# Kernel tuning notes

Measured on AMD Instinct MI355X. Metric: run time of the kernel, lower is better.

Reference implementation:

```python
import jax, jax.numpy as jnp
import numpy as np

HQ, HK, D = 16, 4, 64
WINDOW = 1024  # sliding-window left size; right=0 (causal)
GATE_CH = 12
RMS_EPS = 1e-8


def rms_norm(x):
    return x * jax.lax.rsqrt(jnp.mean(x * x, axis=-1, keepdims=True) + RMS_EPS)


def apply_rope(x, cos, sin):
    # x: [B,T,H,D]; cos/sin: [T,D//2] broadcast to [1,T,1,D//2]
    x1, x2 = jnp.split(x, 2, axis=-1)
    c = cos[None, :, None, :]
    s = sin[None, :, None, :]
    return jnp.concatenate([x1 * c - x2 * s, x1 * s + x2 * c], axis=-1)


def setup_inputs() -> dict:
    key = jax.random.key(0)
    ks = jax.random.split(key, 7)
    B, T, E = 2, 2048, HQ * D
    x = jax.random.normal(ks[0], (B, T, E), jnp.float32)
    value_embeds = jax.random.normal(ks[1], (B, T, HK * D), jnp.float32)
    # rope cache: angles for half the head dim
    inv_freq = 1.0 / (10000.0 ** (jnp.arange(D // 2, dtype=jnp.float32) / (D // 2)))
    ang = jnp.arange(T, dtype=jnp.float32)[:, None] * inv_freq[None, :]
    rope_cos = jnp.cos(ang)
    rope_sin = jnp.sin(ang)
    std = (3.0 ** 0.5) * (E ** -0.5)
    w_qkv = jax.random.uniform(ks[2], ((HQ + 2 * HK) * D, E), jnp.float32, -std, std)
    w_gate = jax.random.normal(ks[3], (HK, GATE_CH), jnp.float32) * 0.02
    w_o = jax.random.normal(ks[4], (E, E), jnp.float32) * 0.02
    return {"x": x, "value_embeds": value_embeds, "rope_cos": rope_cos,
            "rope_sin": rope_sin, "w_qkv": w_qkv, "w_gate": w_gate, "w_o": w_o}


def reference(x, value_embeds, rope_cos, rope_sin, w_qkv, w_gate, w_o):
    B, T, E = x.shape
    groups = HQ // HK
    qkv = jnp.einsum('bte,fe->btf', x, w_qkv).reshape(B, T, HQ + 2 * HK, D)
    q = qkv[:, :, :HQ, :]
    k = qkv[:, :, HQ:HQ + HK, :]
    v = qkv[:, :, HQ + HK:, :]
    # value-embedding gating
    ve = value_embeds.reshape(B, T, HK, D)
    gate = 3.0 * jax.nn.sigmoid(jnp.einsum('btc,hc->bth', x[..., :GATE_CH], w_gate))
    v = v + gate[..., None] * ve
    # rope + qk-norm
    q = rms_norm(apply_rope(q, rope_cos, rope_sin))
    k = rms_norm(apply_rope(k, rope_cos, rope_sin))
    # GQA: repeat kv heads
    k_rep = jnp.repeat(k, groups, axis=2)  # [B,T,HQ,D]
    v_rep = jnp.repeat(v, groups, axis=2)
    scale = 1.0 / jnp.sqrt(jnp.float32(D))
    scores = jnp.einsum('bqhd,bkhd->bhqk', q, k_rep) * scale
    i = jnp.arange(T)[:, None]
    j = jnp.arange(T)[None, :]
    mask = (j <= i) & (j >= i - WINDOW)  # causal + sliding window
    scores = jnp.where(mask[None, None], scores, jnp.float32(-1e30))
    attn = jax.nn.softmax(scores, axis=-1)
    out = jnp.einsum('bhqk,bkhd->bqhd', attn, v_rep).reshape(B, T, E)
    out = jnp.einsum('bte,fe->btf', out, w_o)
    return out
```

## Files before the change

### kernel.cpp

```cpp
#include <hip/hip_runtime.h>
#include <math.h>

#define T_LEN 2048
#define NB 2
#define E_DIM 1024
#define F_DIM 1536
#define HQn 16
#define HKn 4
#define Dh 64
#define WIN 1024
#define GATE_CH 12
#define PS 72

typedef unsigned short u16;
typedef __attribute__((ext_vector_type(8))) short bf16x8;
typedef __attribute__((ext_vector_type(4))) short bf16x4;
typedef __attribute__((ext_vector_type(4))) float f32x4;

#if __has_builtin(__builtin_amdgcn_mfma_f32_16x16x16bf16_1k)
#define MFMA16(A, B, C) __builtin_amdgcn_mfma_f32_16x16x16bf16_1k(A, B, C, 0, 0, 0)
#elif __has_builtin(__builtin_amdgcn_mfma_f32_16x16x16_bf16)
#define MFMA16(A, B, C) __builtin_amdgcn_mfma_f32_16x16x16_bf16(A, B, C, 0, 0, 0)
#else
static __device__ __forceinline__ f32x4 mfma16_asm(bf16x4 a, bf16x4 b, f32x4 c) {
  f32x4 d;
  asm volatile("s_nop 1\n\tv_mfma_f32_16x16x16_bf16 %0, %1, %2, %3\n\ts_nop 7\n\ts_nop 7"
               : "=v"(d) : "v"(a), "v"(b), "v"(c));
  return d;
}
#define MFMA16(A, B, C) mfma16_asm(A, B, C)
#endif

__device__ __forceinline__ u16 f2bf(float f) {
  union { float f; unsigned int u; } v; v.f = f;
  unsigned int u = v.u + 0x7FFF + ((v.u >> 16) & 1);
  return (u16)(u >> 16);
}
__device__ __forceinline__ float bf2f(u16 h) {
  union { unsigned int u; float f; } v; v.u = ((unsigned int)h) << 16;
  return v.f;
}
__device__ __forceinline__ void async_copy16(const void* g, void* l) {
  __builtin_amdgcn_global_load_lds(
      (const __attribute__((address_space(1))) unsigned int*)g,
      (__attribute__((address_space(3))) unsigned int*)l, 16, 0, 0);
}

__global__ __launch_bounds__(256) void cvt_all(
    const float4* __restrict__ x, const float4* __restrict__ wqkv,
    const float4* __restrict__ wo, uint2* __restrict__ xb,
    uint2* __restrict__ wqb, uint2* __restrict__ wob)
{
  int blk = blockIdx.x;
  const float4* in; uint2* out; int i;
  if (blk < 4096)       { in = x;    out = xb;  i = blk * 256 + threadIdx.x; }
  else if (blk < 5632)  { in = wqkv; out = wqb; i = (blk - 4096) * 256 + threadIdx.x; }
  else                  { in = wo;   out = wob; i = (blk - 5632) * 256 + threadIdx.x; }
  float4 v = in[i];
  uint2 o;
  o.x = (unsigned)f2bf(v.x) | ((unsigned)f2bf(v.y) << 16);
  o.y = (unsigned)f2bf(v.z) | ((unsigned)f2bf(v.w) << 16);
  out[i] = o;
}

template<int STORE_BF16>
__global__ __launch_bounds__(256) void gemm_bf16(
    const u16* __restrict__ A, const u16* __restrict__ B,
    void* __restrict__ Cv, int M, int N, int K)
{
  __shared__ u16 As[128 * 32];
  __shared__ u16 Bs[128 * 32];
  const int tid = threadIdx.x;
  const int wave = tid >> 6, lane = tid & 63;
  const int quad = lane >> 4, lanelow = lane & 15;
  const int row0 = blockIdx.x * 128;
  const int col0 = blockIdx.y * 128;
  const int wm = (wave >> 1) * 64, wn = (wave & 1) * 64;

  f32x4 acc[4][4];
#pragma unroll
  for (int i = 0; i < 4; ++i)
#pragma unroll
    for (int j = 0; j < 4; ++j) acc[i][j] = (f32x4){0.f, 0.f, 0.f, 0.f};

  const int r1 = wave * 16 + (lane >> 2);
  const int c1 = (lane & 3) * 8;

  for (int k0 = 0; k0 < K; k0 += 32) {
    __syncthreads();
    async_copy16(A + (size_t)(row0 + r1) * K + k0 + c1,      &As[r1 * 32 + c1]);
    async_copy16(A + (size_t)(row0 + r1 + 64) * K + k0 + c1, &As[(r1 + 64) * 32 + c1]);
    async_copy16(B + (size_t)(col0 + r1) * K + k0 + c1,      &Bs[r1 * 32 + c1]);
    async_copy16(B + (size_t)(col0 + r1 + 64) * K + k0 + c1, &Bs[(r1 + 64) * 32 + c1]);
    __syncthreads();

    bf16x8 a[4], b[4];
#pragma unroll
    for (int i = 0; i < 4; ++i)
      a[i] = *(const bf16x8*)&As[(wm + i * 16 + lanelow) * 32 + quad * 8];
#pragma unroll
    for (int j = 0; j < 4; ++j)
      b[j] = *(const bf16x8*)&Bs[(wn + j * 16 + lanelow) * 32 + quad * 8];
#pragma unroll
    for (int i = 0; i < 4; ++i)
#pragma unroll
      for (int j = 0; j < 4; ++j)
        acc[i][j] = __builtin_amdgcn_mfma_f32_16x16x32_bf16(a[i], b[j], acc[i][j], 0, 0, 0);
  }

#pragma unroll
  for (int i = 0; i < 4; ++i)
#pragma unroll
    for (int j = 0; j < 4; ++j) {
      int r = row0 + wm + i * 16 + quad * 4;
      int c = col0 + wn + j * 16 + lanelow;
#pragma unroll
      for (int reg = 0; reg < 4; ++reg) {
        if (STORE_BF16)
          ((u16*)Cv)[(size_t)(r + reg) * N + c] = f2bf(acc[i][j][reg]);
        else
          ((float*)Cv)[(size_t)(r + reg) * N + c] = acc[i][j][reg];
      }
    }
}

__global__ __launch_bounds__(256) void postproc_bf(
    const u16* __restrict__ qkv, const float* __restrict__ x,
    const float* __restrict__ ve, const float* __restrict__ rcos,
    const float* __restrict__ rsin, const float* __restrict__ wg,
    u16* __restrict__ qa, u16* __restrict__ ka, u16* __restrict__ va)
{
  const int token = blockIdx.x;
  const int t = token & (T_LEN - 1);
  const int tid = threadIdx.x;
  const int wave = tid >> 6, lane = tid & 63;
  __shared__ float gate[HKn];
  if (tid < HKn) {
    float g = 0.f;
#pragma unroll
    for (int c = 0; c < GATE_CH; ++c)
      g += x[(size_t)token * E_DIM + c] * wg[tid * GATE_CH + c];
    gate[tid] = 3.f / (1.f + __expf(-g));
  }
  __syncthreads();
  const int half = lane & 31;
  for (int vi = wave; vi < HQn + HKn; vi += 4) {
    const u16* p = qkv + (size_t)token * F_DIM + vi * Dh;
    float c = rcos[t * 32 + half], s = rsin[t * 32 + half];
    float x1 = bf2f(p[half]), x2 = bf2f(p[half + 32]);
    float y = (lane < 32) ? (x1 * c - x2 * s) : (x1 * s + x2 * c);
    float ss = y * y;
#pragma unroll
    for (int o = 32; o; o >>= 1) ss += __shfl_xor(ss, o, 64);
    float v = y * rsqrtf(ss * (1.f / Dh) + 1e-8f);
    if (vi < HQn)
      qa[((size_t)token * HQn + vi) * Dh + lane] = f2bf(v * 0.1803368801f);
    else
      ka[((size_t)token * HKn + (vi - HQn)) * Dh + lane] = f2bf(v);
  }
  {
    float g = gate[tid >> 6];
    size_t vidx = (size_t)token * (HKn * Dh) + tid;
    va[vidx] = f2bf(bf2f(qkv[(size_t)token * F_DIM + (HQn + HKn) * Dh + tid]) + g * ve[vidx]);
  }
}

__global__ __launch_bounds__(256) void transpose_v(
    const u16* __restrict__ va, u16* __restrict__ vt)
{
  __shared__ u16 tile[64][PS];
  const int bhk = blockIdx.y;
  const int b = bhk >> 2, hk = bhk & 3;
  const int t0 = blockIdx.x * 64;
  const int tid = threadIdx.x;
#pragma unroll
  for (int p = 0; p < 2; ++p) {
    int s = tid + p * 256;
    int r = s >> 3, seg = s & 7;
    *(uint4*)&tile[r][seg * 8] =
        *(const uint4*)(va + ((size_t)(b * T_LEN + t0 + r) * HKn + hk) * Dh + seg * 8);
  }
  __syncthreads();
#pragma unroll
  for (int p = 0; p < 2; ++p) {
    int s = tid + p * 256;
    int d = s >> 3, seg = s & 7;
    u16 tmp[8];
#pragma unroll
    for (int e = 0; e < 8; ++e) tmp[e] = tile[seg * 8 + e][d];
    *(uint4*)(vt + ((size_t)bhk * Dh + d) * T_LEN + t0 + seg * 8) = *(uint4*)tmp;
  }
}

__global__ __launch_bounds__(256) void attn_mfma(
    const u16* __restrict__ qa, const u16* __restrict__ ka,
    const u16* __restrict__ vt_g, u16* __restrict__ att)
{
  __shared__ u16 Ks[2][64 * PS];
  __shared__ u16 Vt[2][64 * PS];
  const int qt = blockIdx.x, h = blockIdx.y, b = blockIdx.z;
  const int hk = h >> 2;
  const int qb = qt * 128;
  const int tid = threadIdx.x;
  const int wave = tid >> 6, lane = tid & 63;
  const int quad = lane >> 4, lanelow = lane & 15;

  bf16x8 aQ[2][2];
#pragma unroll
  for (int hh = 0; hh < 2; ++hh)
#pragma unroll
    for (int kk = 0; kk < 2; ++kk)
      aQ[hh][kk] = *(const bf16x8*)(qa +
          ((size_t)(b * T_LEN + qb + wave * 32 + hh * 16 + lanelow) * HQn + h) * Dh +
          kk * 32 + quad * 8);

  f32x4 O[4][2];
  float l[2] = {0.f, 0.f};
#pragma unroll
  for (int dt = 0; dt < 4; ++dt)
#pragma unroll
    for (int hh = 0; hh < 2; ++hh) O[dt][hh] = (f32x4){0.f, 0.f, 0.f, 0.f};

  const int i_lo = qb + wave * 32, i_hi = i_lo + 31;
  const int kt0 = (qt >= 8) ? qt * 2 - 16 : 0;
  const int kt1 = qt * 2 + 1;

  const int sr0 = tid >> 3,           sc0 = (tid & 7) * 8;
  const int sr1 = (tid + 256) >> 3,   sc1 = ((tid + 256) & 7) * 8;
  const u16* kg = ka + (size_t)(b * T_LEN) * (HKn * Dh) + hk * Dh;
  const u16* vg = vt_g + (size_t)(b * HKn + hk) * Dh * T_LEN;

  {
    const int kb = kt0 * 64;
    uint4 k0 = *(const uint4*)(kg + (size_t)(kb + sr0) * (HKn * Dh) + sc0);
    uint4 k1 = *(const uint4*)(kg + (size_t)(kb + sr1) * (HKn * Dh) + sc1);
    uint4 v0 = *(const uint4*)(vg + (size_t)sr0 * T_LEN + kb + sc0);
    uint4 v1 = *(const uint4*)(vg + (size_t)sr1 * T_LEN + kb + sc1);
    *(uint4*)&Ks[0][sr0 * PS + sc0] = k0;
    *(uint4*)&Ks[0][sr1 * PS + sc1] = k1;
    *(uint4*)&Vt[0][sr0 * PS + sc0] = v0;
    *(uint4*)&Vt[0][sr1 * PS + sc1] = v1;
  }

  for (int kt = kt0; kt <= kt1; ++kt) {
    const int buf = (kt - kt0) & 1;
    const int kb = kt * 64;
    uint4 k0, k1, v0, v1;
    const bool more = (kt < kt1);
    if (more) {
      const int nb = kb + 64;
      k0 = *(const uint4*)(kg + (size_t)(nb + sr0) * (HKn * Dh) + sc0);
      k1 = *(const uint4*)(kg + (size_t)(nb + sr1) * (HKn * Dh) + sc1);
      v0 = *(const uint4*)(vg + (size_t)sr0 * T_LEN + nb + sc0);
      v1 = *(const uint4*)(vg + (size_t)sr1 * T_LEN + nb + sc1);
    }
    __syncthreads();

    const bool active = (kb <= i_hi) && (kb + 63 >= i_lo - WIN);
    if (active) {
      f32x4 St[4][2];
#pragma unroll
      for (int jt = 0; jt < 4; ++jt) {
        bf16x8 aK0 = *(const bf16x8*)&Ks[buf][(jt * 16 + lanelow) * PS + quad * 8];
        bf16x8 aK1 = *(const bf16x8*)&Ks[buf][(jt * 16 + lanelow) * PS + 32 + quad * 8];
#pragma unroll
        for (int hh = 0; hh < 2; ++hh) {
          f32x4 acc = (f32x4){-12.f, -12.f, -12.f, -12.f};
          acc = __builtin_amdgcn_mfma_f32_16x16x32_bf16(aK0, aQ[hh][0], acc, 0, 0, 0);
          acc = __builtin_amdgcn_mfma_f32_16x16x32_bf16(aK1, aQ[hh][1], acc, 0, 0, 0);
          St[jt][hh] = acc;
        }
      }
      const bool need_mask = (kb + 63 > i_lo) || (kb < i_hi - WIN);
      if (need_mask) {
#pragma unroll
        for (int jt = 0; jt < 4; ++jt)
#pragma unroll
          for (int hh = 0; hh < 2; ++hh)
#pragma unroll
            for (int rr = 0; rr < 4; ++rr) {
              int ig = i_lo + hh * 16 + lanelow;
              int jg = kb + jt * 16 + quad * 4 + rr;
              if (jg > ig || jg < ig - WIN) St[jt][hh][rr] = -1e30f;
            }
      }
      bf16x4 Pt[4][2];
#pragma unroll
      for (int jt = 0; jt < 4; ++jt)
#pragma unroll
        for (int hh = 0; hh < 2; ++hh) {
          float p0 = __builtin_amdgcn_exp2f(St[jt][hh][0]);
          float p1 = __builtin_amdgcn_exp2f(St[jt][hh][1]);
          float p2 = __builtin_amdgcn_exp2f(St[jt][hh][2]);
          float p3 = __builtin_amdgcn_exp2f(St[jt][hh][3]);
          l[hh] += (p0 + p1) + (p2 + p3);
          bf16x4 pk;
          pk[0] = (short)f2bf(p0); pk[1] = (short)f2bf(p1);
          pk[2] = (short)f2bf(p2); pk[3] = (short)f2bf(p3);
          Pt[jt][hh] = pk;
        }
#pragma unroll
      for (int dt = 0; dt < 4; ++dt)
#pragma unroll
        for (int jt = 0; jt < 4; ++jt) {
          bf16x4 aV = *(const bf16x4*)&Vt[buf][(dt * 16 + lanelow) * PS + jt * 16 + quad * 4];
#pragma unroll
          for (int hh = 0; hh < 2; ++hh)
            O[dt][hh] = MFMA16(aV, Pt[jt][hh], O[dt][hh]);
        }
    }
    if (more) {
      const int nbuf = buf ^ 1;
      *(uint4*)&Ks[nbuf][sr0 * PS + sc0] = k0;
      *(uint4*)&Ks[nbuf][sr1 * PS + sc1] = k1;
      *(uint4*)&Vt[nbuf][sr0 * PS + sc0] = v0;
      *(uint4*)&Vt[nbuf][sr1 * PS + sc1] = v1;
    }
  }

#pragma unroll
  for (int hh = 0; hh < 2; ++hh) {
    float s = l[hh];
    s += __shfl_xor(s, 16, 64);
    s += __shfl_xor(s, 32, 64);
    float inv = 1.f / s;
    int qg = qb + wave * 32 + hh * 16 + lanelow;
    u16* obase = att + (size_t)(b * T_LEN + qg) * E_DIM + h * Dh;
#pragma unroll
    for (int dt = 0; dt < 4; ++dt) {
      bf16x4 ov;
      ov[0] = (short)f2bf(O[dt][hh][0] * inv);
      ov[1] = (short)f2bf(O[dt][hh][1] * inv);
      ov[2] = (short)f2bf(O[dt][hh][2] * inv);
      ov[3] = (short)f2bf(O[dt][hh][3] * inv);
      *(bf16x4*)(obase + dt * 16 + quad * 4) = ov;
    }
  }
}

extern "C" void kernel_launch(void* const* d_in, const int* in_sizes, int n_in,
                              void* d_out, int out_size, void* d_ws, size_t ws_size,
                              hipStream_t stream)
{
  const float* x    = (const float*)d_in[0];
  const float* ve   = (const float*)d_in[1];
  const float* rc   = (const float*)d_in[2];
  const float* rs   = (const float*)d_in[3];
  const float* wqkv = (const float*)d_in[4];
  const float* wg   = (const float*)d_in[5];
  const float* wo   = (const float*)d_in[6];
  float* out = (float*)d_out;

  char* ws = (char*)d_ws;
  u16* x_bf    = (u16*)(ws);
  u16* v_t     = x_bf;
  u16* wqkv_bf = (u16*)(ws + 8388608);
  u16* wo_bf   = (u16*)(ws + 11534336);
  u16* qkv_bf  = (u16*)(ws + 13631488);
  u16* att     = qkv_bf;
  u16* q_att   = (u16*)(ws + 26214400);
  u16* k_att   = (u16*)(ws + 34603008);
  u16* v_att   = (u16*)(ws + 36700160);

  cvt_all<<<6656, 256, 0, stream>>>((const float4*)x, (const float4*)wqkv,
                                    (const float4*)wo, (uint2*)x_bf,
                                    (uint2*)wqkv_bf, (uint2*)wo_bf);
  gemm_bf16<1><<<dim3(32, 12), 256, 0, stream>>>(x_bf, wqkv_bf, qkv_bf, 4096, F_DIM, E_DIM);
  postproc_bf<<<NB * T_LEN, 256, 0, stream>>>(qkv_bf, x, ve, rc, rs, wg, q_att, k_att, v_att);
  transpose_v<<<dim3(32, 8), 256, 0, stream>>>(v_att, v_t);
  attn_mfma<<<dim3(T_LEN / 128, HQn, NB), 256, 0, stream>>>(q_att, k_att, v_t, att);
  gemm_bf16<0><<<dim3(32, 8), 256, 0, stream>>>(att, wo_bf, out, 4096, E_DIM, E_DIM);
}
```

Baseline: 194.6 us.

## Shrink attention query tile to 64 and use smaller GEMM tiles for occupancy

```diff
diff --git a/kernel.cpp b/kernel.cpp
--- a/kernel.cpp
+++ b/kernel.cpp
@@ -13,6 +13,7 @@
 #define PS 72
 
 typedef unsigned short u16;
+typedef unsigned int u32;
 typedef __attribute__((ext_vector_type(8))) short bf16x8;
 typedef __attribute__((ext_vector_type(4))) short bf16x4;
 typedef __attribute__((ext_vector_type(4))) float f32x4;
@@ -40,6 +41,10 @@
   union { unsigned int u; float f; } v; v.u = ((unsigned int)h) << 16;
   return v.f;
 }
+__device__ __forceinline__ u32 pack_bf2(float hi, float lo) {
+  union { float f; u32 u; } a, b; a.f = hi; b.f = lo;
+  return __builtin_amdgcn_perm(a.u + 0x8000u, b.u + 0x8000u, 0x07060302u);
+}
 __device__ __forceinline__ void async_copy16(const void* g, void* l) {
   __builtin_amdgcn_global_load_lds(
       (const __attribute__((address_space(1))) unsigned int*)g,
@@ -63,55 +68,60 @@
   out[i] = o;
 }
 
-template<int STORE_BF16>
+template<int BM, int BN, int STORE_BF16>
 __global__ __launch_bounds__(256) void gemm_bf16(
     const u16* __restrict__ A, const u16* __restrict__ B,
     void* __restrict__ Cv, int M, int N, int K)
 {
-  __shared__ u16 As[128 * 32];
-  __shared__ u16 Bs[128 * 32];
+  constexpr int MI = BM / 32, NJ = BN / 32;
+  __shared__ u16 As[BM * 32];
+  __shared__ u16 Bs[BN * 32];
   const int tid = threadIdx.x;
   const int wave = tid >> 6, lane = tid & 63;
   const int quad = lane >> 4, lanelow = lane & 15;
-  const int row0 = blockIdx.x * 128;
-  const int col0 = blockIdx.y * 128;
-  const int wm = (wave >> 1) * 64, wn = (wave & 1) * 64;
-
-  f32x4 acc[4][4];
-#pragma unroll
-  for (int i = 0; i < 4; ++i)
-#pragma unroll
-    for (int j = 0; j < 4; ++j) acc[i][j] = (f32x4){0.f, 0.f, 0.f, 0.f};
+  const int row0 = blockIdx.x * BM;
+  const int col0 = blockIdx.y * BN;
+  const int wm = (wave >> 1) * (BM / 2), wn = (wave & 1) * (BN / 2);
+
+  f32x4 acc[MI][NJ];
+#pragma unroll
+  for (int i = 0; i < MI; ++i)
+#pragma unroll
+    for (int j = 0; j < NJ; ++j) acc[i][j] = (f32x4){0.f, 0.f, 0.f, 0.f};
 
   const int r1 = wave * 16 + (lane >> 2);
   const int c1 = (lane & 3) * 8;
 
   for (int k0 = 0; k0 < K; k0 += 32) {
     __syncthreads();
-    async_copy16(A + (size_t)(row0 + r1) * K + k0 + c1,      &As[r1 * 32 + c1]);
-    async_copy16(A + (size_t)(row0 + r1 + 64) * K + k0 + c1, &As[(r1 + 64) * 32 + c1]);
-    async_copy16(B + (size_t)(col0 + r1) * K + k0 + c1,      &Bs[r1 * 32 + c1]);
-    async_copy16(B + (size_t)(col0 + r1 + 64) * K + k0 + c1, &Bs[(r1 + 64) * 32 + c1]);
+#pragma unroll
+    for (int p = 0; p < BM / 64; ++p)
+      async_copy16(A + (size_t)(row0 + r1 + p * 64) * K + k0 + c1,
+                   &As[(r1 + p * 64) * 32 + c1]);
+#pragma unroll
+    for (int p = 0; p < BN / 64; ++p)
+      async_copy16(B + (size_t)(col0 + r1 + p * 64) * K + k0 + c1,
+                   &Bs[(r1 + p * 64) * 32 + c1]);
     __syncthreads();
 
-    bf16x8 a[4], b[4];
-#pragma unroll
-    for (int i = 0; i < 4; ++i)
+    bf16x8 a[MI], b[NJ];
+#pragma unroll
+    for (int i = 0; i < MI; ++i)
       a[i] = *(const bf16x8*)&As[(wm + i * 16 + lanelow) * 32 + quad * 8];
 #pragma unroll
-    for (int j = 0; j < 4; ++j)
+    for (int j = 0; j < NJ; ++j)
       b[j] = *(const bf16x8*)&Bs[(wn + j * 16 + lanelow) * 32 + quad * 8];
 #pragma unroll
-    for (int i = 0; i < 4; ++i)
-#pragma unroll
-      for (int j = 0; j < 4; ++j)
+    for (int i = 0; i < MI; ++i)
+#pragma unroll
+      for (int j = 0; j < NJ; ++j)
         acc[i][j] = __builtin_amdgcn_mfma_f32_16x16x32_bf16(a[i], b[j], acc[i][j], 0, 0, 0);
   }
 
 #pragma unroll
-  for (int i = 0; i < 4; ++i)
-#pragma unroll
-    for (int j = 0; j < 4; ++j) {
+  for (int i = 0; i < MI; ++i)
+#pragma unroll
+    for (int j = 0; j < NJ; ++j) {
       int r = row0 + wm + i * 16 + quad * 4;
       int c = col0 + wn + j * 16 + lanelow;
 #pragma unroll
@@ -200,33 +210,28 @@
   __shared__ u16 Vt[2][64 * PS];
   const int qt = blockIdx.x, h = blockIdx.y, b = blockIdx.z;
   const int hk = h >> 2;
-  const int qb = qt * 128;
+  const int qb = qt * 64;
   const int tid = threadIdx.x;
   const int wave = tid >> 6, lane = tid & 63;
   const int quad = lane >> 4, lanelow = lane & 15;
 
-  bf16x8 aQ[2][2];
-#pragma unroll
-  for (int hh = 0; hh < 2; ++hh)
-#pragma unroll
-    for (int kk = 0; kk < 2; ++kk)
-      aQ[hh][kk] = *(const bf16x8*)(qa +
-          ((size_t)(b * T_LEN + qb + wave * 32 + hh * 16 + lanelow) * HQn + h) * Dh +
-          kk * 32 + quad * 8);
-
-  f32x4 O[4][2];
-  float l[2] = {0.f, 0.f};
-#pragma unroll
-  for (int dt = 0; dt < 4; ++dt)
-#pragma unroll
-    for (int hh = 0; hh < 2; ++hh) O[dt][hh] = (f32x4){0.f, 0.f, 0.f, 0.f};
-
-  const int i_lo = qb + wave * 32, i_hi = i_lo + 31;
-  const int kt0 = (qt >= 8) ? qt * 2 - 16 : 0;
-  const int kt1 = qt * 2 + 1;
-
-  const int sr0 = tid >> 3,           sc0 = (tid & 7) * 8;
-  const int sr1 = (tid + 256) >> 3,   sc1 = ((tid + 256) & 7) * 8;
+  bf16x8 aQ[2];
+#pragma unroll
+  for (int kk = 0; kk < 2; ++kk)
+    aQ[kk] = *(const bf16x8*)(qa +
+        ((size_t)(b * T_LEN + qb + wave * 16 + lanelow) * HQn + h) * Dh +
+        kk * 32 + quad * 8);
+
+  f32x4 O[4];
+  float l = 0.f;
+#pragma unroll
+  for (int dt = 0; dt < 4; ++dt) O[dt] = (f32x4){0.f, 0.f, 0.f, 0.f};
+
+  const int kt0 = (qt >= 16) ? qt - 16 : 0;
+  const int kt1 = qt;
+
+  const int sr0 = tid >> 3,         sc0 = (tid & 7) * 8;
+  const int sr1 = (tid + 256) >> 3, sc1 = ((tid + 256) & 7) * 8;
   const u16* kg = ka + (size_t)(b * T_LEN) * (HKn * Dh) + hk * Dh;
   const u16* vg = vt_g + (size_t)(b * HKn + hk) * Dh * T_LEN;
 
@@ -256,59 +261,55 @@
     }
     __syncthreads();
 
-    const bool active = (kb <= i_hi) && (kb + 63 >= i_lo - WIN);
-    if (active) {
-      f32x4 St[4][2];
+    f32x4 St[4];
+#pragma unroll
+    for (int jt = 0; jt < 4; ++jt) {
+      bf16x8 aK0 = *(const bf16x8*)&Ks[buf][(jt * 16 + lanelow) * PS + quad * 8];
+      bf16x8 aK1 = *(const bf16x8*)&Ks[buf][(jt * 16 + lanelow) * PS + 32 + quad * 8];
+      f32x4 acc = (f32x4){-12.f, -12.f, -12.f, -12.f};
+      acc = __builtin_amdgcn_mfma_f32_16x16x32_bf16(aK0, aQ[0], acc, 0, 0, 0);
+      acc = __builtin_amdgcn_mfma_f32_16x16x32_bf16(aK1, aQ[1], acc, 0, 0, 0);
+      St[jt] = acc;
+    }
+    if (kt == kt1) {
+#pragma unroll
+      for (int jt = 0; jt < 4; ++jt)
+#pragma unroll
+        for (int rr = 0; rr < 4; ++rr) {
+          int ig = qb + wave * 16 + lanelow;
+          int jg = kb + jt * 16 + quad * 4 + rr;
+          if (jg > ig) St[jt][rr] = -1e30f;
+        }
+    } else if (kt == kt0 && qt >= 16) {
+#pragma unroll
+      for (int jt = 0; jt < 4; ++jt)
+#pragma unroll
+        for (int rr = 0; rr < 4; ++rr) {
+          int ig = qb + wave * 16 + lanelow;
+          int jg = kb + jt * 16 + quad * 4 + rr;
+          if (jg < ig - WIN) St[jt][rr] = -1e30f;
+        }
+    }
+    bf16x4 Pt[4];
+#pragma unroll
+    for (int jt = 0; jt < 4; ++jt) {
+      float p0 = __builtin_amdgcn_exp2f(St[jt][0]);
+      float p1 = __builtin_amdgcn_exp2f(St[jt][1]);
+      float p2 = __builtin_amdgcn_exp2f(St[jt][2]);
+      float p3 = __builtin_amdgcn_exp2f(St[jt][3]);
+      l += (p0 + p1) + (p2 + p3);
+      union { uint2 u; bf16x4 v; } pu;
+      pu.u.x = pack_bf2(p1, p0);
+      pu.u.y = pack_bf2(p3, p2);
+      Pt[jt] = pu.v;
+    }
+#pragma unroll
+    for (int dt = 0; dt < 4; ++dt)
 #pragma unroll
       for (int jt = 0; jt < 4; ++jt) {
-        bf16x8 aK0 = *(const bf16x8*)&Ks[buf][(jt * 16 + lanelow) * PS + quad * 8];
-        bf16x8 aK1 = *(const bf16x8*)&Ks[buf][(jt * 16 + lanelow) * PS + 32 + quad * 8];
-#pragma unroll
-        for (int hh = 0; hh < 2; ++hh) {
-          f32x4 acc = (f32x4){-12.f, -12.f, -12.f, -12.f};
-          acc = __builtin_amdgcn_mfma_f32_16x16x32_bf16(aK0, aQ[hh][0], acc, 0, 0, 0);
-          acc = __builtin_amdgcn_mfma_f32_16x16x32_bf16(aK1, aQ[hh][1], acc, 0, 0, 0);
-          St[jt][hh] = acc;
-        }
+        bf16x4 aV = *(const bf16x4*)&Vt[buf][(dt * 16 + lanelow) * PS + jt * 16 + quad * 4];
+        O[dt] = MFMA16(aV, Pt[jt], O[dt]);
       }
-      const bool need_mask = (kb + 63 > i_lo) || (kb < i_hi - WIN);
-      if (need_mask) {
-#pragma unroll
-        for (int jt = 0; jt < 4; ++jt)
-#pragma unroll
-          for (int hh = 0; hh < 2; ++hh)
-#pragma unroll
-            for (int rr = 0; rr < 4; ++rr) {
-              int ig = i_lo + hh * 16 + lanelow;
-              int jg = kb + jt * 16 + quad * 4 + rr;
-              if (jg > ig || jg < ig - WIN) St[jt][hh][rr] = -1e30f;
-            }
-      }
-      bf16x4 Pt[4][2];
-#pragma unroll
-      for (int jt = 0; jt < 4; ++jt)
-#pragma unroll
-        for (int hh = 0; hh < 2; ++hh) {
-          float p0 = __builtin_amdgcn_exp2f(St[jt][hh][0]);
-          float p1 = __builtin_amdgcn_exp2f(St[jt][hh][1]);
-          float p2 = __builtin_amdgcn_exp2f(St[jt][hh][2]);
-          float p3 = __builtin_amdgcn_exp2f(St[jt][hh][3]);
-          l[hh] += (p0 + p1) + (p2 + p3);
-          bf16x4 pk;
-          pk[0] = (short)f2bf(p0); pk[1] = (short)f2bf(p1);
-          pk[2] = (short)f2bf(p2); pk[3] = (short)f2bf(p3);
-          Pt[jt][hh] = pk;
-        }
-#pragma unroll
-      for (int dt = 0; dt < 4; ++dt)
-#pragma unroll
-        for (int jt = 0; jt < 4; ++jt) {
-          bf16x4 aV = *(const bf16x4*)&Vt[buf][(dt * 16 + lanelow) * PS + jt * 16 + quad * 4];
-#pragma unroll
-          for (int hh = 0; hh < 2; ++hh)
-            O[dt][hh] = MFMA16(aV, Pt[jt][hh], O[dt][hh]);
-        }
-    }
     if (more) {
       const int nbuf = buf ^ 1;
       *(uint4*)&Ks[nbuf][sr0 * PS + sc0] = k0;
@@ -318,21 +319,20 @@
     }
   }
 
-#pragma unroll
-  for (int hh = 0; hh < 2; ++hh) {
-    float s = l[hh];
+  {
+    float s = l;
     s += __shfl_xor(s, 16, 64);
     s += __shfl_xor(s, 32, 64);
     float inv = 1.f / s;
-    int qg = qb + wave * 32 + hh * 16 + lanelow;
+    int qg = qb + wave * 16 + lanelow;
     u16* obase = att + (size_t)(b * T_LEN + qg) * E_DIM + h * Dh;
 #pragma unroll
     for (int dt = 0; dt < 4; ++dt) {
       bf16x4 ov;
-      ov[0] = (short)f2bf(O[dt][hh][0] * inv);
-      ov[1] = (short)f2bf(O[dt][hh][1] * inv);
-      ov[2] = (short)f2bf(O[dt][hh][2] * inv);
-      ov[3] = (short)f2bf(O[dt][hh][3] * inv);
+      ov[0] = (short)f2bf(O[dt][0] * inv);
+      ov[1] = (short)f2bf(O[dt][1] * inv);
+      ov[2] = (short)f2bf(O[dt][2] * inv);
+      ov[3] = (short)f2bf(O[dt][3] * inv);
       *(bf16x4*)(obase + dt * 16 + quad * 4) = ov;
     }
   }
@@ -365,9 +365,9 @@
   cvt_all<<<6656, 256, 0, stream>>>((const float4*)x, (const float4*)wqkv,
                                     (const float4*)wo, (uint2*)x_bf,
                                     (uint2*)wqkv_bf, (uint2*)wo_bf);
-  gemm_bf16<1><<<dim3(32, 12), 256, 0, stream>>>(x_bf, wqkv_bf, qkv_bf, 4096, F_DIM, E_DIM);
+  gemm_bf16<128, 64, 1><<<dim3(32, 24), 256, 0, stream>>>(x_bf, wqkv_bf, qkv_bf, 4096, F_DIM, E_DIM);
   postproc_bf<<<NB * T_LEN, 256, 0, stream>>>(qkv_bf, x, ve, rc, rs, wg, q_att, k_att, v_att);
   transpose_v<<<dim3(32, 8), 256, 0, stream>>>(v_att, v_t);
-  attn_mfma<<<dim3(T_LEN / 128, HQn, NB), 256, 0, stream>>>(q_att, k_att, v_t, att);
-  gemm_bf16<0><<<dim3(32, 8), 256, 0, stream>>>(att, wo_bf, out, 4096, E_DIM, E_DIM);
-}
+  attn_mfma<<<dim3(T_LEN / 64, HQn, NB), 256, 0, stream>>>(q_att, k_att, v_t, att);
+  gemm_bf16<64, 64, 0><<<dim3(64, 16), 256, 0, stream>>>(att, wo_bf, out, 4096, E_DIM, E_DIM);
+}
```

After: 181.6 us. 1.07x faster.
